# Optimization experiments

Measured on AMD Instinct MI355X. Metric: run time of the kernel, lower is better.

The kernel has to match this reference:

```python
import jax, jax.numpy as jnp
import numpy as np

N, E, IN, H, D = 100000, 1600000, 128, 4, 64
NEG_SLOPE = 0.2
K_APPNP, ALPHA = 5, 0.5
BN_EPS = 1e-5


def setup_inputs() -> dict:
    key = jax.random.key(0)
    ks = jax.random.split(key, 12)
    return {
        'node_feats': jax.random.normal(ks[0], (N, IN), jnp.float32),
        'src': jax.random.randint(ks[1], (E,), 0, N, jnp.int32),
        'dst': jax.random.randint(ks[2], (E,), 0, N, jnp.int32),
        'W_fc': jax.random.normal(ks[3], (IN, H * D), jnp.float32) * (1.0 / np.sqrt(IN)),
        'attn_l': jax.random.normal(ks[4], (H, D), jnp.float32) * 0.1,
        'attn_r': jax.random.normal(ks[5], (H, D), jnp.float32) * 0.1,
        'W_res_gat': jax.random.normal(ks[6], (IN, H * D), jnp.float32) * (1.0 / np.sqrt(IN)),
        'gat_bias': jax.random.normal(ks[7], (H * D,), jnp.float32) * 0.01,
        'conv_w': jax.random.normal(ks[8], (1, H), jnp.float32) * 0.5,
        'conv_b': jax.random.normal(ks[9], (1,), jnp.float32) * 0.01,
        'W_res': jax.random.normal(ks[10], (D, IN), jnp.float32) * (1.0 / np.sqrt(IN)),
        'b_res': jax.random.normal(ks[11], (D,), jnp.float32) * 0.01,
        'gamma': jnp.ones((D,), jnp.float32),
        'beta': jnp.zeros((D,), jnp.float32),
    }


def reference(node_feats, src, dst, W_fc, attn_l, attn_r, W_res_gat, gat_bias,
              conv_w, conv_b, W_res, b_res, gamma, beta):
    # ---- GATConv (4 heads, residual, relu) ----
    feat = (node_feats @ W_fc).reshape(N, H, D)            # (N,H,D)
    el = jnp.einsum('nhd,hd->nh', feat, attn_l)            # (N,H)
    er = jnp.einsum('nhd,hd->nh', feat, attn_r)
    e = jax.nn.leaky_relu(el[src] + er[dst], NEG_SLOPE)    # (E,H)
    # edge softmax over incoming edges of each dst node
    emax = jax.ops.segment_max(e, dst, num_segments=N)     # (N,H)
    emax = jnp.where(jnp.isfinite(emax), emax, 0.0)
    ee = jnp.exp(e - emax[dst])                            # (E,H)
    denom = jax.ops.segment_sum(ee, dst, num_segments=N)   # (N,H)
    a = ee / jnp.maximum(denom[dst], 1e-9)                 # (E,H)
    msg = feat[src] * a[..., None]                         # (E,H,D)
    rst = jax.ops.segment_sum(msg, dst, num_segments=N)    # (N,H,D)
    resval = (node_feats @ W_res_gat).reshape(N, H, D)
    rst = jax.nn.relu(rst + resval + gat_bias.reshape(1, H, D))
    # ---- Conv1d (heads -> 1, kernel_size=1) then flatten ----
    h = jnp.einsum('nhd,oh->nod', rst, conv_w) + conv_b[None, :, None]
    h = h.reshape(N, D)
    # ---- APPNP (k=5, alpha=0.5), symmetric deg^{-1/2} norm (in-degree, clamp 1) ----
    deg = jax.ops.segment_sum(jnp.ones((E,), jnp.float32), dst, num_segments=N)
    norm = jnp.power(jnp.maximum(deg, 1.0), -0.5)[:, None]  # (N,1)
    h0 = h
    for _ in range(K_APPNP):
        h = jax.ops.segment_sum((h * norm)[src], dst, num_segments=N) * norm
        h = (1.0 - ALPHA) * h + ALPHA * h0
    # ---- residual linear + relu ----
    h = h + jax.nn.relu(node_feats @ W_res.T + b_res)
    # ---- BatchNorm1d (batch stats, affine) ----
    mu = h.mean(axis=0)
    var = h.var(axis=0)
    return (h - mu) * jax.lax.rsqrt(var + BN_EPS) * gamma + beta
```

## Files before the change

### kernel.cpp

```cpp
#include <hip/hip_runtime.h>
#include <math.h>

#define NN 100000
#define NE 1600000
#define NEG_SLOPE 0.2f

typedef __attribute__((ext_vector_type(8))) short bf16x8;
typedef __attribute__((ext_vector_type(4))) float f32x4;
typedef __attribute__((ext_vector_type(2))) float f32x2;

__device__ __forceinline__ float b2f(unsigned short u) {
  union { unsigned u; float f; } c; c.u = ((unsigned)u) << 16; return c.f;
}
__device__ __forceinline__ unsigned short f2b(float x) {
  union { float f; unsigned u; } c; c.f = x;
  unsigned r = c.u + 0x7FFFu + ((c.u >> 16) & 1u);
  return (unsigned short)(r >> 16);
}
__device__ __forceinline__ void fma4(float4& acc, float s, const float4& b) {
  acc.x = fmaf(s, b.x, acc.x);
  acc.y = fmaf(s, b.y, acc.y);
  acc.z = fmaf(s, b.z, acc.z);
  acc.w = fmaf(s, b.w, acc.w);
}

__global__ __launch_bounds__(256) void k_zero(int* __restrict__ p, int nwords) {
  int i = blockIdx.x * 256 + threadIdx.x;
  if (i < nwords) p[i] = 0;
}

__global__ void k_zrow(unsigned short* __restrict__ a, unsigned short* __restrict__ b) {
  int i = threadIdx.x;
  a[(size_t)NN * 64 + i] = 0;
  b[(size_t)NN * 64 + i] = 0;
}

__global__ __launch_bounds__(256) void k_cast(const float* __restrict__ A, unsigned short* __restrict__ Ab) {
  int i = blockIdx.x * 256 + threadIdx.x;
  int i4 = i * 4;
  if (i4 < NN * 128) {
    float4 v = *(const float4*)&A[i4];
    ushort4 o; o.x = f2b(v.x); o.y = f2b(v.y); o.z = f2b(v.z); o.w = f2b(v.w);
    *(ushort4*)&Ab[i4] = o;
  }
}

__global__ __launch_bounds__(256) void k_deg(const int* __restrict__ dst, int* __restrict__ deg) {
  int i = blockIdx.x * 256 + threadIdx.x;
  if (i < NE) atomicAdd(&deg[dst[i]], 1);
}

__global__ __launch_bounds__(256) void k_alloc(const int* __restrict__ deg, int* __restrict__ row_start,
                                               int* __restrict__ counter, float* __restrict__ nrm) {
  int i = blockIdx.x * 256 + threadIdx.x;
  if (i < NN) {
    row_start[i] = atomicAdd(counter, deg[i]);
    nrm[i] = rsqrtf(fmaxf((float)deg[i], 1.0f));
  }
}

__global__ __launch_bounds__(256) void k_scatter(const int* __restrict__ src, const int* __restrict__ dst,
                                                 const int* __restrict__ row_start, int* __restrict__ cursor,
                                                 int* __restrict__ csr_src) {
  int i = blockIdx.x * 256 + threadIdx.x;
  if (i < NE) {
    int n = dst[i];
    int p = atomicAdd(&cursor[n], 1);
    csr_src[row_start[n] + p] = src[i];
  }
}

__global__ __launch_bounds__(256) void k_prepw(const float* __restrict__ W_fc, const float* __restrict__ al,
                                               const float* __restrict__ ar, float* __restrict__ w) {
  int o = blockIdx.x * 256 + threadIdx.x;
  if (o >= 1024) return;
  int side = o >> 9;
  int h = (o >> 7) & 3;
  int k = o & 127;
  const float* a = side ? ar : al;
  float s = 0.f;
  for (int d = 0; d < 64; ++d) s += W_fc[k * 256 + h * 64 + d] * a[h * 64 + d];
  w[(side * 4 + h) * 128 + k] = s;
}

__global__ __launch_bounds__(256) void k_elr2(const float* __restrict__ X, const float* __restrict__ w,
                                              float* __restrict__ el, float* __restrict__ er) {
  int n = blockIdx.x * 32 + (threadIdx.x >> 3);
  int p = threadIdx.x & 7;
  if (n >= NN) return;
  const float4* xr = (const float4*)(X + (size_t)n * 128);
  const float4* wr = (const float4*)(w + p * 128);
  float s = 0.f;
#pragma unroll
  for (int i = 0; i < 32; ++i) {
    float4 x = xr[i], ww = wr[i];
    s += x.x * ww.x + x.y * ww.y + x.z * ww.z + x.w * ww.w;
  }
  if (p < 4) el[n * 4 + p] = s;
  else er[n * 4 + (p - 4)] = s;
}

__global__ __launch_bounds__(256) void k_prepB(const float* __restrict__ W_fc, const float* __restrict__ W_rg,
                                               unsigned short* __restrict__ Bp) {
  int y = blockIdx.y;
  const float* Bsrc = (y >> 1) ? W_rg : W_fc;
  int colbase = (y & 1) * 128;
  for (int e = blockIdx.x * 256 + threadIdx.x; e < 16384; e += 2048) {
    int n = e & 127, k = e >> 7;
    int p = colbase + n;
    int d = p >> 2, hh = p & 3;
    float v = Bsrc[k * 256 + hh * 64 + d];
    int nt = n >> 4, nn = n & 15, kt = k >> 5, quad = (k >> 3) & 3, j = k & 7;
    Bp[(size_t)y * 16384 + ((kt * 8 + nt) * 64 + quad * 16 + nn) * 8 + j] = f2b(v);
  }
}

__global__ __launch_bounds__(256) void k_gemm_mfma(const unsigned short* __restrict__ Abf,
                                                   const unsigned short* __restrict__ Bp,
                                                   unsigned* __restrict__ feat8u,
                                                   unsigned short* __restrict__ resval2) {
  __shared__ unsigned short Al[128 * 136];
  __shared__ unsigned short Bl[8192];
  int tid = threadIdx.x;
  int half = blockIdx.y >> 1;
  int colbase = (blockIdx.y & 1) * 128;
  int row0 = blockIdx.x * 128;
#pragma unroll
  for (int i = 0; i < 8; ++i) {
    int c = tid + i * 256;
    int row = c >> 4, part = c & 15;
    int gr = row0 + row; if (gr > NN - 1) gr = NN - 1;
    *(uint4*)&Al[row * 136 + part * 8] = *(const uint4*)&Abf[(size_t)gr * 128 + part * 8];
  }
  {
    const uint4* srcb = (const uint4*)(Bp + (size_t)blockIdx.y * 16384);
    uint4* dst4 = (uint4*)Bl;
#pragma unroll
    for (int i = 0; i < 4; ++i) dst4[tid + i * 256] = srcb[tid + i * 256];
  }
  __syncthreads();
  int w = tid >> 6, lane = tid & 63;
  int quad = lane >> 4, l16 = lane & 15;
  f32x4 acc[8][2];
#pragma unroll
  for (int rt = 0; rt < 8; ++rt)
#pragma unroll
    for (int c = 0; c < 2; ++c) acc[rt][c] = (f32x4){0.f, 0.f, 0.f, 0.f};
#pragma unroll
  for (int kh = 0; kh < 2; ++kh) {
    if (kh == 1) {
      __syncthreads();
      const uint4* srcb = (const uint4*)(Bp + (size_t)blockIdx.y * 16384 + 8192);
      uint4* dst4 = (uint4*)Bl;
#pragma unroll
      for (int i = 0; i < 4; ++i) dst4[tid + i * 256] = srcb[tid + i * 256];
      __syncthreads();
    }
#pragma unroll
    for (int ktl = 0; ktl < 2; ++ktl) {
      int kt = kh * 2 + ktl;
      bf16x8 b0 = *(const bf16x8*)&Bl[((ktl * 8 + w * 2 + 0) * 64 + lane) * 8];
      bf16x8 b1 = *(const bf16x8*)&Bl[((ktl * 8 + w * 2 + 1) * 64 + lane) * 8];
      int kb = kt * 32 + quad * 8;
#pragma unroll
      for (int rt = 0; rt < 8; ++rt) {
        bf16x8 a = *(const bf16x8*)&Al[(rt * 16 + l16) * 136 + kb];
        acc[rt][0] = __builtin_amdgcn_mfma_f32_16x16x32_bf16(b0, a, acc[rt][0], 0, 0, 0);
        acc[rt][1] = __builtin_amdgcn_mfma_f32_16x16x32_bf16(b1, a, acc[rt][1], 0, 0, 0);
      }
    }
  }
  __syncthreads();
  if (half == 0) {
    unsigned* Cl = (unsigned*)Al;
#pragma unroll
    for (int rt = 0; rt < 8; ++rt)
#pragma unroll
      for (int c = 0; c < 2; ++c) {
        int pk = __builtin_amdgcn_cvt_pk_fp8_f32(acc[rt][c][0], acc[rt][c][1], 0, false);
        pk = __builtin_amdgcn_cvt_pk_fp8_f32(acc[rt][c][2], acc[rt][c][3], pk, true);
        Cl[(rt * 16 + l16) * 36 + (w * 2 + c) * 4 + quad] = (unsigned)pk;
      }
    __syncthreads();
#pragma unroll
    for (int i = 0; i < 4; ++i) {
      int c = tid + i * 256;
      int row = c >> 3, wp = c & 7;
      int m = row0 + row;
      if (m < NN)
        *(uint4*)&feat8u[(size_t)m * 64 + (colbase >> 2) + wp * 4] = *(const uint4*)&Cl[row * 36 + wp * 4];
    }
  } else {
#pragma unroll
    for (int rt = 0; rt < 8; ++rt)
#pragma unroll
      for (int c = 0; c < 2; ++c) {
        int col = (w * 2 + c) * 16 + quad * 4;
        ushort4 o;
        o.x = f2b(acc[rt][c][0]); o.y = f2b(acc[rt][c][1]);
        o.z = f2b(acc[rt][c][2]); o.w = f2b(acc[rt][c][3]);
        *(ushort4*)&Al[(rt * 16 + l16) * 136 + col] = o;
      }
    __syncthreads();
#pragma unroll
    for (int i = 0; i < 8; ++i) {
      int c = tid + i * 256;
      int row = c >> 4, part = c & 15;
      int m = row0 + row;
      if (m < NN)
        *(uint4*)&resval2[(size_t)m * 256 + colbase + part * 8] = *(const uint4*)&Al[row * 136 + part * 8];
    }
  }
}

__global__ __launch_bounds__(256) void k_gemm_nt_bias_relu(const float* __restrict__ A, const float* __restrict__ B,
                                                           const float* __restrict__ bias, float* __restrict__ C) {
  __shared__ float Bl[128][68];
  for (int idx = threadIdx.x; idx < 64 * 128; idx += 256) {
    int d = idx >> 7, k = idx & 127;
    Bl[k][d] = B[d * 128 + k];
  }
  __syncthreads();
  int tx = threadIdx.x & 15, ty = threadIdx.x >> 4;
  int row0 = blockIdx.x * 64 + ty * 4;
  const float* ap[4];
#pragma unroll
  for (int r = 0; r < 4; ++r) ap[r] = A + (size_t)min(row0 + r, NN - 1) * 128;
  float4 acc[4];
#pragma unroll
  for (int r = 0; r < 4; ++r) acc[r] = make_float4(0.f, 0.f, 0.f, 0.f);
#pragma unroll 2
  for (int k0 = 0; k0 < 128; k0 += 4) {
    float4 b0 = *(const float4*)&Bl[k0][tx * 4];
    float4 b1 = *(const float4*)&Bl[k0 + 1][tx * 4];
    float4 b2 = *(const float4*)&Bl[k0 + 2][tx * 4];
    float4 b3 = *(const float4*)&Bl[k0 + 3][tx * 4];
#pragma unroll
    for (int r = 0; r < 4; ++r) {
      float4 a = *(const float4*)(ap[r] + k0);
      fma4(acc[r], a.x, b0); fma4(acc[r], a.y, b1);
      fma4(acc[r], a.z, b2); fma4(acc[r], a.w, b3);
    }
  }
  float4 bv = *(const float4*)&bias[tx * 4];
#pragma unroll
  for (int r = 0; r < 4; ++r) {
    int row = row0 + r;
    if (row < NN) {
      float4 v;
      v.x = fmaxf(acc[r].x + bv.x, 0.f);
      v.y = fmaxf(acc[r].y + bv.y, 0.f);
      v.z = fmaxf(acc[r].z + bv.z, 0.f);
      v.w = fmaxf(acc[r].w + bv.w, 0.f);
      *(float4*)&C[(size_t)row * 64 + tx * 4] = v;
    }
  }
}

__global__ __launch_bounds__(256) void k_gat(const int* __restrict__ row_start, const int* __restrict__ deg,
                                             const int* __restrict__ csr_src, const float* __restrict__ el,
                                             const float* __restrict__ er, const unsigned* __restrict__ feat8u,
                                             const unsigned short* __restrict__ resval2,
                                             const float* __restrict__ gat_bias, const float* __restrict__ conv_w,
                                             const float* __restrict__ conv_b, const float* __restrict__ nrm,
                                             float* __restrict__ h0, unsigned short* __restrict__ hsA) {
  __shared__ int s_src[4][64];
  __shared__ float s_x[4][64][4];
  int wid = threadIdx.x >> 6, lane = threadIdx.x & 63;
  int n = blockIdx.x * 4 + wid;
  if (n >= NN) return;
  int s0 = row_start[n], cnt = deg[n];
  float4 er4 = *(const float4*)&er[n * 4];
  int k = lane & 31, g = lane >> 5;
  unsigned koff = (unsigned)(k << 3);
  f32x2 a01_0 = (f32x2){0.f, 0.f}, a23_0 = (f32x2){0.f, 0.f};
  f32x2 a01_1 = (f32x2){0.f, 0.f}, a23_1 = (f32x2){0.f, 0.f};
  f32x2 den01 = (f32x2){0.f, 0.f}, den23 = (f32x2){0.f, 0.f};
  for (int base = 0; base < cnt; base += 64) {
    int j = base + lane;
    int s = 0;
    float x0 = 0.f, x1 = 0.f, x2 = 0.f, x3 = 0.f;
    if (j < cnt) {
      s = csr_src[s0 + j];
      float4 el4 = *(const float4*)&el[s * 4];
      float e0 = el4.x + er4.x; e0 = (e0 > 0.f) ? e0 : NEG_SLOPE * e0;
      float e1 = el4.y + er4.y; e1 = (e1 > 0.f) ? e1 : NEG_SLOPE * e1;
      float e2 = el4.z + er4.z; e2 = (e2 > 0.f) ? e2 : NEG_SLOPE * e2;
      float e3 = el4.w + er4.w; e3 = (e3 > 0.f) ? e3 : NEG_SLOPE * e3;
      x0 = __expf(e0); x1 = __expf(e1); x2 = __expf(e2); x3 = __expf(e3);
    }
    s_src[wid][lane] = s;
    *(float4*)&s_x[wid][lane][0] = make_float4(x0, x1, x2, x3);
    int m = cnt - base; if (m > 64) m = 64;
    int mr = (m + 3) & ~3;
    for (int t = 0; t < mr; t += 4) {
      int sA = s_src[wid][t + g];
      int sB = s_src[wid][t + 2 + g];
      float4 xA = *(const float4*)&s_x[wid][t + g][0];
      float4 xB = *(const float4*)&s_x[wid][t + 2 + g][0];
      uint2 fA = *(const uint2*)((const char*)feat8u + (((unsigned)sA << 8) + koff));
      uint2 fB = *(const uint2*)((const char*)feat8u + (((unsigned)sB << 8) + koff));
      f32x2 xa01 = (f32x2){xA.x, xA.y}, xa23 = (f32x2){xA.z, xA.w};
      f32x2 xb01 = (f32x2){xB.x, xB.y}, xb23 = (f32x2){xB.z, xB.w};
      den01 += xa01; den01 += xb01;
      den23 += xa23; den23 += xb23;
      f32x2 lo, hi;
      lo = __builtin_amdgcn_cvt_pk_f32_fp8((int)fA.x, false);
      hi = __builtin_amdgcn_cvt_pk_f32_fp8((int)fA.x, true);
      a01_0 += xa01 * lo; a23_0 += xa23 * hi;
      lo = __builtin_amdgcn_cvt_pk_f32_fp8((int)fA.y, false);
      hi = __builtin_amdgcn_cvt_pk_f32_fp8((int)fA.y, true);
      a01_1 += xa01 * lo; a23_1 += xa23 * hi;
      lo = __builtin_amdgcn_cvt_pk_f32_fp8((int)fB.x, false);
      hi = __builtin_amdgcn_cvt_pk_f32_fp8((int)fB.x, true);
      a01_0 += xb01 * lo; a23_0 += xb23 * hi;
      lo = __builtin_amdgcn_cvt_pk_f32_fp8((int)fB.y, false);
      hi = __builtin_amdgcn_cvt_pk_f32_fp8((int)fB.y, true);
      a01_1 += xb01 * lo; a23_1 += xb23 * hi;
    }
  }
  den01[0] += __shfl_xor(den01[0], 32, 64);
  den01[1] += __shfl_xor(den01[1], 32, 64);
  den23[0] += __shfl_xor(den23[0], 32, 64);
  den23[1] += __shfl_xor(den23[1], 32, 64);
  float i0 = 1.f / fmaxf(den01[0], 1e-9f);
  float i1 = 1.f / fmaxf(den01[1], 1e-9f);
  float i2 = 1.f / fmaxf(den23[0], 1e-9f);
  float i3 = 1.f / fmaxf(den23[1], 1e-9f);
  a01_0[0] += __shfl_xor(a01_0[0], 32, 64);
  a01_0[1] += __shfl_xor(a01_0[1], 32, 64);
  a23_0[0] += __shfl_xor(a23_0[0], 32, 64);
  a23_0[1] += __shfl_xor(a23_0[1], 32, 64);
  a01_1[0] += __shfl_xor(a01_1[0], 32, 64);
  a01_1[1] += __shfl_xor(a01_1[1], 32, 64);
  a23_1[0] += __shfl_xor(a23_1[0], 32, 64);
  a23_1[1] += __shfl_xor(a23_1[1], 32, 64);
  if (lane < 32) {
    int d0 = k << 1;
    uint4 rv = *(const uint4*)&resval2[(size_t)n * 256 + ((unsigned)k << 3)];
    float2 bb0 = *(const float2*)&gat_bias[d0];
    float2 bb1 = *(const float2*)&gat_bias[64 + d0];
    float2 bb2 = *(const float2*)&gat_bias[128 + d0];
    float2 bb3 = *(const float2*)&gat_bias[192 + d0];
    float cb = conv_b[0];
    float cw0 = conv_w[0], cw1 = conv_w[1], cw2 = conv_w[2], cw3 = conv_w[3];
    float t, hm0 = cb, hm1 = cb;
    t = fmaf(a01_0[0], i0, b2f((unsigned short)(rv.x & 0xffffu)) + bb0.x); t = fmaxf(t, 0.f); hm0 = fmaf(cw0, t, hm0);
    t = fmaf(a01_0[1], i1, b2f((unsigned short)(rv.x >> 16)) + bb1.x);     t = fmaxf(t, 0.f); hm0 = fmaf(cw1, t, hm0);
    t = fmaf(a23_0[0], i2, b2f((unsigned short)(rv.y & 0xffffu)) + bb2.x); t = fmaxf(t, 0.f); hm0 = fmaf(cw2, t, hm0);
    t = fmaf(a23_0[1], i3, b2f((unsigned short)(rv.y >> 16)) + bb3.x);     t = fmaxf(t, 0.f); hm0 = fmaf(cw3, t, hm0);
    t = fmaf(a01_1[0], i0, b2f((unsigned short)(rv.z & 0xffffu)) + bb0.y); t = fmaxf(t, 0.f); hm1 = fmaf(cw0, t, hm1);
    t = fmaf(a01_1[1], i1, b2f((unsigned short)(rv.z >> 16)) + bb1.y);     t = fmaxf(t, 0.f); hm1 = fmaf(cw1, t, hm1);
    t = fmaf(a23_1[0], i2, b2f((unsigned short)(rv.w & 0xffffu)) + bb2.y); t = fmaxf(t, 0.f); hm1 = fmaf(cw2, t, hm1);
    t = fmaf(a23_1[1], i3, b2f((unsigned short)(rv.w >> 16)) + bb3.y);     t = fmaxf(t, 0.f); hm1 = fmaf(cw3, t, hm1);
    float nn_ = nrm[n];
    size_t o = (size_t)n * 64 + d0;
    *(float2*)&h0[o] = make_float2(hm0, hm1);
    ushort2 hs; hs.x = f2b(hm0 * nn_); hs.y = f2b(hm1 * nn_);
    *(ushort2*)&hsA[o] = hs;
  }
}

__device__ __forceinline__ void gather_accum(const int* __restrict__ row_start, const int* __restrict__ deg,
                                             const int* __restrict__ csr_src,
                                             const unsigned short* __restrict__ hs_in,
                                             int n, int wid, int lane,
                                             float& a0, float& a1, float& a2, float& a3) {
  __shared__ int s_src[4][64];
  int s0 = row_start[n], cnt = deg[n];
  int k = lane & 15, g = lane >> 4;
  unsigned koff = (unsigned)(k << 3);
  a0 = 0.f; a1 = 0.f; a2 = 0.f; a3 = 0.f;
  for (int base = 0; base < cnt; base += 64) {
    int j = base + lane;
    s_src[wid][lane] = (j < cnt) ? csr_src[s0 + j] : NN;
    int m = cnt - base; if (m > 64) m = 64;
    int mr = (m + 7) & ~7;
    for (int t = 0; t < mr; t += 8) {
      int sA = s_src[wid][t + g];
      int sB = s_src[wid][t + 4 + g];
      uint2 uA = *(const uint2*)((const char*)hs_in + (((unsigned)sA << 7) + koff));
      uint2 uB = *(const uint2*)((const char*)hs_in + (((unsigned)sB << 7) + koff));
      a0 += __uint_as_float(uA.x << 16);
      a1 += __uint_as_float(uA.x & 0xFFFF0000u);
      a2 += __uint_as_float(uA.y << 16);
      a3 += __uint_as_float(uA.y & 0xFFFF0000u);
      a0 += __uint_as_float(uB.x << 16);
      a1 += __uint_as_float(uB.x & 0xFFFF0000u);
      a2 += __uint_as_float(uB.y << 16);
      a3 += __uint_as_float(uB.y & 0xFFFF0000u);
    }
  }
  a0 += __shfl_xor(a0, 16, 64); a1 += __shfl_xor(a1, 16, 64);
  a2 += __shfl_xor(a2, 16, 64); a3 += __shfl_xor(a3, 16, 64);
  a0 += __shfl_xor(a0, 32, 64); a1 += __shfl_xor(a1, 32, 64);
  a2 += __shfl_xor(a2, 32, 64); a3 += __shfl_xor(a3, 32, 64);
}

__global__ __launch_bounds__(256) void k_gather_mid(const int* __restrict__ row_start, const int* __restrict__ deg,
                                                    const int* __restrict__ csr_src,
                                                    const unsigned short* __restrict__ hs_in,
                                                    const float* __restrict__ nrm, const float* __restrict__ h0,
                                                    unsigned short* __restrict__ hs_out) {
  int wid = threadIdx.x >> 6, lane = threadIdx.x & 63;
  int n = blockIdx.x * 4 + wid;
  if (n >= NN) return;
  float a0, a1, a2, a3;
  gather_accum(row_start, deg, csr_src, hs_in, n, wid, lane, a0, a1, a2, a3);
  if (lane < 16) {
    size_t o = (size_t)n * 64 + (lane << 2);
    float nn_ = nrm[n];
    float4 h4 = *(const float4*)&h0[o];
    float hn = 0.5f * nn_;
    float v0 = fmaf(hn, a0, 0.5f * h4.x) * nn_;
    float v1 = fmaf(hn, a1, 0.5f * h4.y) * nn_;
    float v2 = fmaf(hn, a2, 0.5f * h4.z) * nn_;
    float v3 = fmaf(hn, a3, 0.5f * h4.w) * nn_;
    ushort4 ov; ov.x = f2b(v0); ov.y = f2b(v1); ov.z = f2b(v2); ov.w = f2b(v3);
    *(ushort4*)&hs_out[o] = ov;
  }
}

__global__ __launch_bounds__(256) void k_gather_last(const int* __restrict__ row_start, const int* __restrict__ deg,
                                                     const int* __restrict__ csr_src,
                                                     const unsigned short* __restrict__ hs_in,
                                                     const float* __restrict__ nrm,
                                                     const float* __restrict__ res2,
                                                     float* h0io) {
  int wid = threadIdx.x >> 6, lane = threadIdx.x & 63;
  int n = blockIdx.x * 4 + wid;
  if (n >= NN) return;
  float a0, a1, a2, a3;
  gather_accum(row_start, deg, csr_src, hs_in, n, wid, lane, a0, a1, a2, a3);
  if (lane < 16) {
    size_t o = (size_t)n * 64 + (lane << 2);
    float nn_ = nrm[n];
    float4 h4 = *(const float4*)&h0io[o];
    float4 r4 = *(const float4*)&res2[o];
    float hn = 0.5f * nn_;
    float4 v;
    v.x = fmaf(hn, a0, 0.5f * h4.x) + r4.x;
    v.y = fmaf(hn, a1, 0.5f * h4.y) + r4.y;
    v.z = fmaf(hn, a2, 0.5f * h4.z) + r4.z;
    v.w = fmaf(hn, a3, 0.5f * h4.w) + r4.w;
    *(float4*)&h0io[o] = v;
  }
}

__global__ __launch_bounds__(256) void k_finred(const float* __restrict__ hfin, float* __restrict__ bn) {
  __shared__ float s1[256], s2[256];
  int d = threadIdx.x & 63;
  int rb = blockIdx.x * 64;
  float sum = 0.f, sq = 0.f;
  for (int r = threadIdx.x >> 6; r < 64; r += 4) {
    int n = rb + r;
    if (n < NN) {
      float v = hfin[(size_t)n * 64 + d];
      sum += v; sq += v * v;
    }
  }
  s1[threadIdx.x] = sum; s2[threadIdx.x] = sq;
  __syncthreads();
  if (threadIdx.x < 128) { s1[threadIdx.x] += s1[threadIdx.x + 128]; s2[threadIdx.x] += s2[threadIdx.x + 128]; }
  __syncthreads();
  if (threadIdx.x < 64) {
    atomicAdd(&bn[d], s1[threadIdx.x] + s1[threadIdx.x + 64]);
    atomicAdd(&bn[64 + d], s2[threadIdx.x] + s2[threadIdx.x + 64]);
  }
}

__global__ void k_bnstats(const float* __restrict__ bn, const float* __restrict__ gamma,
                          const float* __restrict__ beta, float* __restrict__ bns) {
  int d = threadIdx.x;
  float mu = bn[d] * (1.0f / NN);
  float var = fmaxf(bn[64 + d] * (1.0f / NN) - mu * mu, 0.f);
  float sc = rsqrtf(var + 1e-5f) * gamma[d];
  bns[d] = sc;
  bns[64 + d] = beta[d] - mu * sc;
}

__global__ __launch_bounds__(256) void k_bnapply(const float* __restrict__ h, const float* __restrict__ bns,
                                                 float* __restrict__ out) {
  int i = blockIdx.x * 256 + threadIdx.x;
  if (i < NN * 64) {
    int d = i & 63;
    out[i] = fmaf(h[i], bns[d], bns[64 + d]);
  }
}

extern "C" void kernel_launch(void* const* d_in, const int* in_sizes, int n_in,
                              void* d_out, int out_size, void* d_ws, size_t ws_size,
                              hipStream_t stream) {
  const float* node_feats = (const float*)d_in[0];
  const int* src = (const int*)d_in[1];
  const int* dst = (const int*)d_in[2];
  const float* W_fc = (const float*)d_in[3];
  const float* attn_l = (const float*)d_in[4];
  const float* attn_r = (const float*)d_in[5];
  const float* W_res_gat = (const float*)d_in[6];
  const float* gat_bias = (const float*)d_in[7];
  const float* conv_w = (const float*)d_in[8];
  const float* conv_b = (const float*)d_in[9];
  const float* W_res = (const float*)d_in[10];
  const float* b_res = (const float*)d_in[11];
  const float* gamma = (const float*)d_in[12];
  const float* beta = (const float*)d_in[13];
  float* out = (float*)d_out;

  char* base = (char*)d_ws;
  size_t off = 0;
  auto alloc = [&](size_t bytes) -> char* {
    char* p = base + off;
    off = (off + bytes + 255) & ~(size_t)255;
    return p;
  };
  unsigned* feat8u        = (unsigned*)alloc((size_t)NN * 256);
  unsigned short* resval2 = (unsigned short*)alloc((size_t)NN * 256 * 2);
  float* res2             = (float*)resval2;
  float* el               = (float*)alloc((size_t)NN * 4 * 4);
  float* er               = (float*)alloc((size_t)NN * 4 * 4);
  float* h0               = (float*)alloc((size_t)NN * 64 * 4);
  unsigned short* Abf     = (unsigned short*)h0;
  unsigned short* hsA     = (unsigned short*)alloc((size_t)(NN + 1) * 64 * 2);
  unsigned short* hsB     = (unsigned short*)alloc((size_t)(NN + 1) * 64 * 2);
  int* csr_src            = (int*)alloc((size_t)NE * 4);
  float* nrm              = (float*)alloc((size_t)NN * 4);
  int* row_start          = (int*)alloc((size_t)NN * 4);
  unsigned short* Bpacked = (unsigned short*)alloc((size_t)4 * 16384 * 2);
  float* w_elr            = (float*)alloc((size_t)8 * 128 * 4);
  size_t zoff = off;
  int* deg                = (int*)alloc((size_t)NN * 4);
  int* cursor             = (int*)alloc((size_t)NN * 4);
  int* counter            = (int*)alloc(256);
  float* bn               = (float*)alloc(256 * 4);
  float* hfin             = h0;

  int zwords = (int)((off - zoff) / 4);
  int gE = (NE + 255) / 256;
  int gN = (NN + 255) / 256;
  int gW = (NN + 3) / 4;
  int gM = (NN + 63) / 64;
  int gV = (NN * 64 + 255) / 256;

  k_zero<<<(zwords + 255) / 256, 256, 0, stream>>>((int*)(base + zoff), zwords);
  k_zrow<<<1, 64, 0, stream>>>(hsA, hsB);
  k_deg<<<gE, 256, 0, stream>>>(dst, deg);
  k_alloc<<<gN, 256, 0, stream>>>(deg, row_start, counter, nrm);
  k_scatter<<<gE, 256, 0, stream>>>(src, dst, row_start, cursor, csr_src);

  k_cast<<<(NN * 128 / 4 + 255) / 256, 256, 0, stream>>>(node_feats, Abf);
  k_prepB<<<dim3(8, 4), 256, 0, stream>>>(W_fc, W_res_gat, Bpacked);
  k_prepw<<<4, 256, 0, stream>>>(W_fc, attn_l, attn_r, w_elr);
  k_gemm_mfma<<<dim3((NN + 127) / 128, 4), 256, 0, stream>>>(Abf, Bpacked, feat8u, resval2);

  k_elr2<<<(NN + 31) / 32, 256, 0, stream>>>(node_feats, w_elr, el, er);
  k_gat<<<gW, 256, 0, stream>>>(row_start, deg, csr_src, el, er, feat8u, resval2,
                                gat_bias, conv_w, conv_b, nrm, h0, hsA);

  k_gemm_nt_bias_relu<<<gM, 256, 0, stream>>>(node_feats, W_res, b_res, res2);

  k_gather_mid<<<gW, 256, 0, stream>>>(row_start, deg, csr_src, hsA, nrm, h0, hsB);
  k_gather_mid<<<gW, 256, 0, stream>>>(row_start, deg, csr_src, hsB, nrm, h0, hsA);
  k_gather_mid<<<gW, 256, 0, stream>>>(row_start, deg, csr_src, hsA, nrm, h0, hsB);
  k_gather_mid<<<gW, 256, 0, stream>>>(row_start, deg, csr_src, hsB, nrm, h0, hsA);
  k_gather_last<<<gW, 256, 0, stream>>>(row_start, deg, csr_src, hsA, nrm, res2, hfin);

  k_finred<<<gM, 256, 0, stream>>>(hfin, bn);
  k_bnstats<<<1, 64, 0, stream>>>(bn, gamma, beta, bn + 128);
  k_bnapply<<<gV, 256, 0, stream>>>(hfin, bn + 128, out);
}
```

Before: 781.4 us.

## Widen gather loads to 16B, read bf16 h0 in APPNP, reuse bf16 input

The GAT and APPNP gather loops now give each lane a 16-byte row load covering more columns, so more edges are in flight per wave-iteration, with one extra cross-lane shuffle step per accumulator. The middle APPNP steps read a bf16 copy of norm-scaled h0 (hs0) instead of fp32 h0, using the identity h0 = hs0/norm folded into a nn^2 factor, which halves that read traffic. The attention-logit kernel reads the bf16 cast of node_feats instead of the fp32 input. Reading h0 and the input in bf16 adds some rounding error in exchange for less bandwidth.

```diff
diff --git a/kernel.cpp b/kernel.cpp
--- a/kernel.cpp
+++ b/kernel.cpp
@@ -29,10 +29,12 @@
   if (i < nwords) p[i] = 0;
 }
 
-__global__ void k_zrow(unsigned short* __restrict__ a, unsigned short* __restrict__ b) {
+__global__ void k_zrow(unsigned short* __restrict__ a, unsigned short* __restrict__ b,
+                       unsigned short* __restrict__ c) {
   int i = threadIdx.x;
   a[(size_t)NN * 64 + i] = 0;
   b[(size_t)NN * 64 + i] = 0;
+  c[(size_t)NN * 64 + i] = 0;
 }
 
 __global__ __launch_bounds__(256) void k_cast(const float* __restrict__ A, unsigned short* __restrict__ Ab) {
@@ -83,18 +85,22 @@
   w[(side * 4 + h) * 128 + k] = s;
 }
 
-__global__ __launch_bounds__(256) void k_elr2(const float* __restrict__ X, const float* __restrict__ w,
+__global__ __launch_bounds__(256) void k_elr2(const unsigned short* __restrict__ X, const float* __restrict__ w,
                                               float* __restrict__ el, float* __restrict__ er) {
   int n = blockIdx.x * 32 + (threadIdx.x >> 3);
   int p = threadIdx.x & 7;
   if (n >= NN) return;
-  const float4* xr = (const float4*)(X + (size_t)n * 128);
+  const uint4* xr = (const uint4*)(X + (size_t)n * 128);
   const float4* wr = (const float4*)(w + p * 128);
   float s = 0.f;
 #pragma unroll
-  for (int i = 0; i < 32; ++i) {
-    float4 x = xr[i], ww = wr[i];
-    s += x.x * ww.x + x.y * ww.y + x.z * ww.z + x.w * ww.w;
+  for (int i = 0; i < 16; ++i) {
+    uint4 x = xr[i];
+    float4 w0 = wr[2 * i], w1 = wr[2 * i + 1];
+    s += __uint_as_float(x.x << 16) * w0.x + __uint_as_float(x.x & 0xFFFF0000u) * w0.y
+       + __uint_as_float(x.y << 16) * w0.z + __uint_as_float(x.y & 0xFFFF0000u) * w0.w
+       + __uint_as_float(x.z << 16) * w1.x + __uint_as_float(x.z & 0xFFFF0000u) * w1.y
+       + __uint_as_float(x.w << 16) * w1.z + __uint_as_float(x.w & 0xFFFF0000u) * w1.w;
   }
   if (p < 4) el[n * 4 + p] = s;
   else er[n * 4 + (p - 4)] = s;
@@ -263,7 +269,7 @@
                                              const unsigned short* __restrict__ resval2,
                                              const float* __restrict__ gat_bias, const float* __restrict__ conv_w,
                                              const float* __restrict__ conv_b, const float* __restrict__ nrm,
-                                             float* __restrict__ h0, unsigned short* __restrict__ hsA) {
+                                             float* __restrict__ h0, unsigned short* __restrict__ hs0o) {
   __shared__ int s_src[4][64];
   __shared__ float s_x[4][64][4];
   int wid = threadIdx.x >> 6, lane = threadIdx.x & 63;
@@ -271,10 +277,11 @@
   if (n >= NN) return;
   int s0 = row_start[n], cnt = deg[n];
   float4 er4 = *(const float4*)&er[n * 4];
-  int k = lane & 31, g = lane >> 5;
-  unsigned koff = (unsigned)(k << 3);
-  f32x2 a01_0 = (f32x2){0.f, 0.f}, a23_0 = (f32x2){0.f, 0.f};
-  f32x2 a01_1 = (f32x2){0.f, 0.f}, a23_1 = (f32x2){0.f, 0.f};
+  int kk = lane & 15, g = lane >> 4;
+  unsigned koff = (unsigned)(kk << 4);
+  f32x2 acc01[4], acc23[4];
+#pragma unroll
+  for (int i = 0; i < 4; ++i) { acc01[i] = (f32x2){0.f, 0.f}; acc23[i] = (f32x2){0.f, 0.f}; }
   f32x2 den01 = (f32x2){0.f, 0.f}, den23 = (f32x2){0.f, 0.f};
   for (int base = 0; base < cnt; base += 64) {
     int j = base + lane;
@@ -294,130 +301,143 @@
     int m = cnt - base; if (m > 64) m = 64;
     int mr = (m + 3) & ~3;
     for (int t = 0; t < mr; t += 4) {
-      int sA = s_src[wid][t + g];
-      int sB = s_src[wid][t + 2 + g];
-      float4 xA = *(const float4*)&s_x[wid][t + g][0];
-      float4 xB = *(const float4*)&s_x[wid][t + 2 + g][0];
-      uint2 fA = *(const uint2*)((const char*)feat8u + (((unsigned)sA << 8) + koff));
-      uint2 fB = *(const uint2*)((const char*)feat8u + (((unsigned)sB << 8) + koff));
-      f32x2 xa01 = (f32x2){xA.x, xA.y}, xa23 = (f32x2){xA.z, xA.w};
-      f32x2 xb01 = (f32x2){xB.x, xB.y}, xb23 = (f32x2){xB.z, xB.w};
-      den01 += xa01; den01 += xb01;
-      den23 += xa23; den23 += xb23;
+      int s_ = s_src[wid][t + g];
+      float4 x4 = *(const float4*)&s_x[wid][t + g][0];
+      uint4 f = *(const uint4*)((const char*)feat8u + (((unsigned)s_ << 8) + koff));
+      f32x2 x01 = (f32x2){x4.x, x4.y}, x23 = (f32x2){x4.z, x4.w};
+      den01 += x01; den23 += x23;
       f32x2 lo, hi;
-      lo = __builtin_amdgcn_cvt_pk_f32_fp8((int)fA.x, false);
-      hi = __builtin_amdgcn_cvt_pk_f32_fp8((int)fA.x, true);
-      a01_0 += xa01 * lo; a23_0 += xa23 * hi;
-      lo = __builtin_amdgcn_cvt_pk_f32_fp8((int)fA.y, false);
-      hi = __builtin_amdgcn_cvt_pk_f32_fp8((int)fA.y, true);
-      a01_1 += xa01 * lo; a23_1 += xa23 * hi;
-      lo = __builtin_amdgcn_cvt_pk_f32_fp8((int)fB.x, false);
-      hi = __builtin_amdgcn_cvt_pk_f32_fp8((int)fB.x, true);
-      a01_0 += xb01 * lo; a23_0 += xb23 * hi;
-      lo = __builtin_amdgcn_cvt_pk_f32_fp8((int)fB.y, false);
-      hi = __builtin_amdgcn_cvt_pk_f32_fp8((int)fB.y, true);
-      a01_1 += xb01 * lo; a23_1 += xb23 * hi;
-    }
-  }
-  den01[0] += __shfl_xor(den01[0], 32, 64);
-  den01[1] += __shfl_xor(den01[1], 32, 64);
-  den23[0] += __shfl_xor(den23[0], 32, 64);
-  den23[1] += __shfl_xor(den23[1], 32, 64);
+      lo = __builtin_amdgcn_cvt_pk_f32_fp8((int)f.x, false);
+      hi = __builtin_amdgcn_cvt_pk_f32_fp8((int)f.x, true);
+      acc01[0] += x01 * lo; acc23[0] += x23 * hi;
+      lo = __builtin_amdgcn_cvt_pk_f32_fp8((int)f.y, false);
+      hi = __builtin_amdgcn_cvt_pk_f32_fp8((int)f.y, true);
+      acc01[1] += x01 * lo; acc23[1] += x23 * hi;
+      lo = __builtin_amdgcn_cvt_pk_f32_fp8((int)f.z, false);
+      hi = __builtin_amdgcn_cvt_pk_f32_fp8((int)f.z, true);
+      acc01[2] += x01 * lo; acc23[2] += x23 * hi;
+      lo = __builtin_amdgcn_cvt_pk_f32_fp8((int)f.w, false);
+      hi = __builtin_amdgcn_cvt_pk_f32_fp8((int)f.w, true);
+      acc01[3] += x01 * lo; acc23[3] += x23 * hi;
+    }
+  }
+  den01[0] += __shfl_xor(den01[0], 16, 64); den01[1] += __shfl_xor(den01[1], 16, 64);
+  den23[0] += __shfl_xor(den23[0], 16, 64); den23[1] += __shfl_xor(den23[1], 16, 64);
+  den01[0] += __shfl_xor(den01[0], 32, 64); den01[1] += __shfl_xor(den01[1], 32, 64);
+  den23[0] += __shfl_xor(den23[0], 32, 64); den23[1] += __shfl_xor(den23[1], 32, 64);
   float i0 = 1.f / fmaxf(den01[0], 1e-9f);
   float i1 = 1.f / fmaxf(den01[1], 1e-9f);
   float i2 = 1.f / fmaxf(den23[0], 1e-9f);
   float i3 = 1.f / fmaxf(den23[1], 1e-9f);
-  a01_0[0] += __shfl_xor(a01_0[0], 32, 64);
-  a01_0[1] += __shfl_xor(a01_0[1], 32, 64);
-  a23_0[0] += __shfl_xor(a23_0[0], 32, 64);
-  a23_0[1] += __shfl_xor(a23_0[1], 32, 64);
-  a01_1[0] += __shfl_xor(a01_1[0], 32, 64);
-  a01_1[1] += __shfl_xor(a01_1[1], 32, 64);
-  a23_1[0] += __shfl_xor(a23_1[0], 32, 64);
-  a23_1[1] += __shfl_xor(a23_1[1], 32, 64);
-  if (lane < 32) {
-    int d0 = k << 1;
-    uint4 rv = *(const uint4*)&resval2[(size_t)n * 256 + ((unsigned)k << 3)];
-    float2 bb0 = *(const float2*)&gat_bias[d0];
-    float2 bb1 = *(const float2*)&gat_bias[64 + d0];
-    float2 bb2 = *(const float2*)&gat_bias[128 + d0];
-    float2 bb3 = *(const float2*)&gat_bias[192 + d0];
+#pragma unroll
+  for (int i = 0; i < 4; ++i) {
+    acc01[i][0] += __shfl_xor(acc01[i][0], 16, 64);
+    acc01[i][1] += __shfl_xor(acc01[i][1], 16, 64);
+    acc23[i][0] += __shfl_xor(acc23[i][0], 16, 64);
+    acc23[i][1] += __shfl_xor(acc23[i][1], 16, 64);
+    acc01[i][0] += __shfl_xor(acc01[i][0], 32, 64);
+    acc01[i][1] += __shfl_xor(acc01[i][1], 32, 64);
+    acc23[i][0] += __shfl_xor(acc23[i][0], 32, 64);
+    acc23[i][1] += __shfl_xor(acc23[i][1], 32, 64);
+  }
+  if (lane < 16) {
+    int d0 = kk << 2;
+    uint4 rv0 = *(const uint4*)&resval2[(size_t)n * 256 + (kk << 4)];
+    uint4 rv1 = *(const uint4*)&resval2[(size_t)n * 256 + (kk << 4) + 8];
+    unsigned short c[16];
+    *(uint4*)&c[0] = rv0; *(uint4*)&c[8] = rv1;
+    float4 b0 = *(const float4*)&gat_bias[d0];
+    float4 b1 = *(const float4*)&gat_bias[64 + d0];
+    float4 b2 = *(const float4*)&gat_bias[128 + d0];
+    float4 b3 = *(const float4*)&gat_bias[192 + d0];
+    float bh0[4] = {b0.x, b0.y, b0.z, b0.w};
+    float bh1[4] = {b1.x, b1.y, b1.z, b1.w};
+    float bh2[4] = {b2.x, b2.y, b2.z, b2.w};
+    float bh3[4] = {b3.x, b3.y, b3.z, b3.w};
     float cb = conv_b[0];
     float cw0 = conv_w[0], cw1 = conv_w[1], cw2 = conv_w[2], cw3 = conv_w[3];
-    float t, hm0 = cb, hm1 = cb;
-    t = fmaf(a01_0[0], i0, b2f((unsigned short)(rv.x & 0xffffu)) + bb0.x); t = fmaxf(t, 0.f); hm0 = fmaf(cw0, t, hm0);
-    t = fmaf(a01_0[1], i1, b2f((unsigned short)(rv.x >> 16)) + bb1.x);     t = fmaxf(t, 0.f); hm0 = fmaf(cw1, t, hm0);
-    t = fmaf(a23_0[0], i2, b2f((unsigned short)(rv.y & 0xffffu)) + bb2.x); t = fmaxf(t, 0.f); hm0 = fmaf(cw2, t, hm0);
-    t = fmaf(a23_0[1], i3, b2f((unsigned short)(rv.y >> 16)) + bb3.x);     t = fmaxf(t, 0.f); hm0 = fmaf(cw3, t, hm0);
-    t = fmaf(a01_1[0], i0, b2f((unsigned short)(rv.z & 0xffffu)) + bb0.y); t = fmaxf(t, 0.f); hm1 = fmaf(cw0, t, hm1);
-    t = fmaf(a01_1[1], i1, b2f((unsigned short)(rv.z >> 16)) + bb1.y);     t = fmaxf(t, 0.f); hm1 = fmaf(cw1, t, hm1);
-    t = fmaf(a23_1[0], i2, b2f((unsigned short)(rv.w & 0xffffu)) + bb2.y); t = fmaxf(t, 0.f); hm1 = fmaf(cw2, t, hm1);
-    t = fmaf(a23_1[1], i3, b2f((unsigned short)(rv.w >> 16)) + bb3.y);     t = fmaxf(t, 0.f); hm1 = fmaf(cw3, t, hm1);
+    float hm[4];
+#pragma unroll
+    for (int i = 0; i < 4; ++i) {
+      float t_, hmv = cb;
+      t_ = fmaf(acc01[i][0], i0, b2f(c[4 * i + 0]) + bh0[i]); t_ = fmaxf(t_, 0.f); hmv = fmaf(cw0, t_, hmv);
+      t_ = fmaf(acc01[i][1], i1, b2f(c[4 * i + 1]) + bh1[i]); t_ = fmaxf(t_, 0.f); hmv = fmaf(cw1, t_, hmv);
+      t_ = fmaf(acc23[i][0], i2, b2f(c[4 * i + 2]) + bh2[i]); t_ = fmaxf(t_, 0.f); hmv = fmaf(cw2, t_, hmv);
+      t_ = fmaf(acc23[i][1], i3, b2f(c[4 * i + 3]) + bh3[i]); t_ = fmaxf(t_, 0.f); hmv = fmaf(cw3, t_, hmv);
+      hm[i] = hmv;
+    }
     float nn_ = nrm[n];
     size_t o = (size_t)n * 64 + d0;
-    *(float2*)&h0[o] = make_float2(hm0, hm1);
-    ushort2 hs; hs.x = f2b(hm0 * nn_); hs.y = f2b(hm1 * nn_);
-    *(ushort2*)&hsA[o] = hs;
-  }
-}
-
-__device__ __forceinline__ void gather_accum(const int* __restrict__ row_start, const int* __restrict__ deg,
-                                             const int* __restrict__ csr_src,
-                                             const unsigned short* __restrict__ hs_in,
-                                             int n, int wid, int lane,
-                                             float& a0, float& a1, float& a2, float& a3) {
+    *(float4*)&h0[o] = make_float4(hm[0], hm[1], hm[2], hm[3]);
+    ushort4 hs;
+    hs.x = f2b(hm[0] * nn_); hs.y = f2b(hm[1] * nn_);
+    hs.z = f2b(hm[2] * nn_); hs.w = f2b(hm[3] * nn_);
+    *(ushort4*)&hs0o[o] = hs;
+  }
+}
+
+__device__ __forceinline__ void gather_accum8(const int* __restrict__ row_start, const int* __restrict__ deg,
+                                              const int* __restrict__ csr_src,
+                                              const unsigned short* __restrict__ hs_in,
+                                              int n, int wid, int lane, float (&a)[8]) {
   __shared__ int s_src[4][64];
   int s0 = row_start[n], cnt = deg[n];
-  int k = lane & 15, g = lane >> 4;
-  unsigned koff = (unsigned)(k << 3);
-  a0 = 0.f; a1 = 0.f; a2 = 0.f; a3 = 0.f;
+  int k = lane & 7, g = lane >> 3;
+  unsigned koff = (unsigned)(k << 4);
+#pragma unroll
+  for (int i = 0; i < 8; ++i) a[i] = 0.f;
   for (int base = 0; base < cnt; base += 64) {
     int j = base + lane;
     s_src[wid][lane] = (j < cnt) ? csr_src[s0 + j] : NN;
     int m = cnt - base; if (m > 64) m = 64;
     int mr = (m + 7) & ~7;
     for (int t = 0; t < mr; t += 8) {
-      int sA = s_src[wid][t + g];
-      int sB = s_src[wid][t + 4 + g];
-      uint2 uA = *(const uint2*)((const char*)hs_in + (((unsigned)sA << 7) + koff));
-      uint2 uB = *(const uint2*)((const char*)hs_in + (((unsigned)sB << 7) + koff));
-      a0 += __uint_as_float(uA.x << 16);
-      a1 += __uint_as_float(uA.x & 0xFFFF0000u);
-      a2 += __uint_as_float(uA.y << 16);
-      a3 += __uint_as_float(uA.y & 0xFFFF0000u);
-      a0 += __uint_as_float(uB.x << 16);
-      a1 += __uint_as_float(uB.x & 0xFFFF0000u);
-      a2 += __uint_as_float(uB.y << 16);
-      a3 += __uint_as_float(uB.y & 0xFFFF0000u);
-    }
-  }
-  a0 += __shfl_xor(a0, 16, 64); a1 += __shfl_xor(a1, 16, 64);
-  a2 += __shfl_xor(a2, 16, 64); a3 += __shfl_xor(a3, 16, 64);
-  a0 += __shfl_xor(a0, 32, 64); a1 += __shfl_xor(a1, 32, 64);
-  a2 += __shfl_xor(a2, 32, 64); a3 += __shfl_xor(a3, 32, 64);
+      int s = s_src[wid][t + g];
+      uint4 u = *(const uint4*)((const char*)hs_in + (((unsigned)s << 7) + koff));
+      a[0] += __uint_as_float(u.x << 16);
+      a[1] += __uint_as_float(u.x & 0xFFFF0000u);
+      a[2] += __uint_as_float(u.y << 16);
+      a[3] += __uint_as_float(u.y & 0xFFFF0000u);
+      a[4] += __uint_as_float(u.z << 16);
+      a[5] += __uint_as_float(u.z & 0xFFFF0000u);
+      a[6] += __uint_as_float(u.w << 16);
+      a[7] += __uint_as_float(u.w & 0xFFFF0000u);
+    }
+  }
+#pragma unroll
+  for (int i = 0; i < 8; ++i) {
+    a[i] += __shfl_xor(a[i], 8, 64);
+    a[i] += __shfl_xor(a[i], 16, 64);
+    a[i] += __shfl_xor(a[i], 32, 64);
+  }
 }
 
 __global__ __launch_bounds__(256) void k_gather_mid(const int* __restrict__ row_start, const int* __restrict__ deg,
                                                     const int* __restrict__ csr_src,
                                                     const unsigned short* __restrict__ hs_in,
-                                                    const float* __restrict__ nrm, const float* __restrict__ h0,
+                                                    const float* __restrict__ nrm,
+                                                    const unsigned short* __restrict__ hs0,
                                                     unsigned short* __restrict__ hs_out) {
   int wid = threadIdx.x >> 6, lane = threadIdx.x & 63;
   int n = blockIdx.x * 4 + wid;
   if (n >= NN) return;
-  float a0, a1, a2, a3;
-  gather_accum(row_start, deg, csr_src, hs_in, n, wid, lane, a0, a1, a2, a3);
-  if (lane < 16) {
-    size_t o = (size_t)n * 64 + (lane << 2);
+  float a[8];
+  gather_accum8(row_start, deg, csr_src, hs_in, n, wid, lane, a);
+  if (lane < 8) {
+    size_t o = (size_t)n * 64 + (lane << 3);
     float nn_ = nrm[n];
-    float4 h4 = *(const float4*)&h0[o];
-    float hn = 0.5f * nn_;
-    float v0 = fmaf(hn, a0, 0.5f * h4.x) * nn_;
-    float v1 = fmaf(hn, a1, 0.5f * h4.y) * nn_;
-    float v2 = fmaf(hn, a2, 0.5f * h4.z) * nn_;
-    float v3 = fmaf(hn, a3, 0.5f * h4.w) * nn_;
-    ushort4 ov; ov.x = f2b(v0); ov.y = f2b(v1); ov.z = f2b(v2); ov.w = f2b(v3);
-    *(ushort4*)&hs_out[o] = ov;
+    float hnn = 0.5f * nn_ * nn_;
+    uint4 z = *(const uint4*)&hs0[o];
+    unsigned zz[4] = {z.x, z.y, z.z, z.w};
+    unsigned short ov[8];
+#pragma unroll
+    for (int i = 0; i < 4; ++i) {
+      float hlo = __uint_as_float(zz[i] << 16);
+      float hhi = __uint_as_float(zz[i] & 0xFFFF0000u);
+      ov[2 * i] = f2b(fmaf(hnn, a[2 * i], 0.5f * hlo));
+      ov[2 * i + 1] = f2b(fmaf(hnn, a[2 * i + 1], 0.5f * hhi));
+    }
+    *(uint4*)&hs_out[o] = *(const uint4*)&ov[0];
   }
 }
 
@@ -430,20 +450,27 @@
   int wid = threadIdx.x >> 6, lane = threadIdx.x & 63;
   int n = blockIdx.x * 4 + wid;
   if (n >= NN) return;
-  float a0, a1, a2, a3;
-  gather_accum(row_start, deg, csr_src, hs_in, n, wid, lane, a0, a1, a2, a3);
-  if (lane < 16) {
-    size_t o = (size_t)n * 64 + (lane << 2);
+  float a[8];
+  gather_accum8(row_start, deg, csr_src, hs_in, n, wid, lane, a);
+  if (lane < 8) {
+    size_t o = (size_t)n * 64 + (lane << 3);
     float nn_ = nrm[n];
-    float4 h4 = *(const float4*)&h0io[o];
-    float4 r4 = *(const float4*)&res2[o];
     float hn = 0.5f * nn_;
-    float4 v;
-    v.x = fmaf(hn, a0, 0.5f * h4.x) + r4.x;
-    v.y = fmaf(hn, a1, 0.5f * h4.y) + r4.y;
-    v.z = fmaf(hn, a2, 0.5f * h4.z) + r4.z;
-    v.w = fmaf(hn, a3, 0.5f * h4.w) + r4.w;
-    *(float4*)&h0io[o] = v;
+    float4 h4a = *(const float4*)&h0io[o];
+    float4 h4b = *(const float4*)&h0io[o + 4];
+    float4 r4a = *(const float4*)&res2[o];
+    float4 r4b = *(const float4*)&res2[o + 4];
+    float4 va, vb;
+    va.x = fmaf(hn, a[0], 0.5f * h4a.x) + r4a.x;
+    va.y = fmaf(hn, a[1], 0.5f * h4a.y) + r4a.y;
+    va.z = fmaf(hn, a[2], 0.5f * h4a.z) + r4a.z;
+    va.w = fmaf(hn, a[3], 0.5f * h4a.w) + r4a.w;
+    vb.x = fmaf(hn, a[4], 0.5f * h4b.x) + r4b.x;
+    vb.y = fmaf(hn, a[5], 0.5f * h4b.y) + r4b.y;
+    vb.z = fmaf(hn, a[6], 0.5f * h4b.z) + r4b.z;
+    vb.w = fmaf(hn, a[7], 0.5f * h4b.w) + r4b.w;
+    *(float4*)&h0io[o] = va;
+    *(float4*)&h0io[o + 4] = vb;
   }
 }
 
@@ -521,6 +548,7 @@
   float* er               = (float*)alloc((size_t)NN * 4 * 4);
   float* h0               = (float*)alloc((size_t)NN * 64 * 4);
   unsigned short* Abf     = (unsigned short*)h0;
+  unsigned short* hs0     = (unsigned short*)alloc((size_t)(NN + 1) * 64 * 2);
   unsigned short* hsA     = (unsigned short*)alloc((size_t)(NN + 1) * 64 * 2);
   unsigned short* hsB     = (unsigned short*)alloc((size_t)(NN + 1) * 64 * 2);
   int* csr_src            = (int*)alloc((size_t)NE * 4);
@@ -543,7 +571,7 @@
   int gV = (NN * 64 + 255) / 256;
 
   k_zero<<<(zwords + 255) / 256, 256, 0, stream>>>((int*)(base + zoff), zwords);
-  k_zrow<<<1, 64, 0, stream>>>(hsA, hsB);
+  k_zrow<<<1, 64, 0, stream>>>(hs0, hsA, hsB);
   k_deg<<<gE, 256, 0, stream>>>(dst, deg);
   k_alloc<<<gN, 256, 0, stream>>>(deg, row_start, counter, nrm);
   k_scatter<<<gE, 256, 0, stream>>>(src, dst, row_start, cursor, csr_src);
@@ -553,17 +581,17 @@
   k_prepw<<<4, 256, 0, stream>>>(W_fc, attn_l, attn_r, w_elr);
   k_gemm_mfma<<<dim3((NN + 127) / 128, 4), 256, 0, stream>>>(Abf, Bpacked, feat8u, resval2);
 
-  k_elr2<<<(NN + 31) / 32, 256, 0, stream>>>(node_feats, w_elr, el, er);
+  k_elr2<<<(NN + 31) / 32, 256, 0, stream>>>(Abf, w_elr, el, er);
   k_gat<<<gW, 256, 0, stream>>>(row_start, deg, csr_src, el, er, feat8u, resval2,
-                                gat_bias, conv_w, conv_b, nrm, h0, hsA);
+                                gat_bias, conv_w, conv_b, nrm, h0, hs0);
 
   k_gemm_nt_bias_relu<<<gM, 256, 0, stream>>>(node_feats, W_res, b_res, res2);
 
-  k_gather_mid<<<gW, 256, 0, stream>>>(row_start, deg, csr_src, hsA, nrm, h0, hsB);
-  k_gather_mid<<<gW, 256, 0, stream>>>(row_start, deg, csr_src, hsB, nrm, h0, hsA);
-  k_gather_mid<<<gW, 256, 0, stream>>>(row_start, deg, csr_src, hsA, nrm, h0, hsB);
-  k_gather_mid<<<gW, 256, 0, stream>>>(row_start, deg, csr_src, hsB, nrm, h0, hsA);
-  k_gather_last<<<gW, 256, 0, stream>>>(row_start, deg, csr_src, hsA, nrm, res2, hfin);
+  k_gather_mid<<<gW, 256, 0, stream>>>(row_start, deg, csr_src, hs0, nrm, hs0, hsA);
+  k_gather_mid<<<gW, 256, 0, stream>>>(row_start, deg, csr_src, hsA, nrm, hs0, hsB);
+  k_gather_mid<<<gW, 256, 0, stream>>>(row_start, deg, csr_src, hsB, nrm, hs0, hsA);
+  k_gather_mid<<<gW, 256, 0, stream>>>(row_start, deg, csr_src, hsA, nrm, hs0, hsB);
+  k_gather_last<<<gW, 256, 0, stream>>>(row_start, deg, csr_src, hsB, nrm, res2, hfin);
 
   k_finred<<<gM, 256, 0, stream>>>(hfin, bn);
   k_bnstats<<<1, 64, 0, stream>>>(bn, gamma, beta, bn + 128);
```

Result: no change. 792.2 us (+1.4%).
